# Performance work log

Hardware: AMD Instinct MI355X
Metric: run time of the kernel (lower is better)

## Reference

```python
import jax, jax.numpy as jnp
import numpy as np

IN_FEATURES = 8192
OUT_FEATURES = 8192
POOL_K = 16
SCALE = 2.0


def setup_inputs() -> dict:
    key = jax.random.key(0)
    k1, k2, k3 = jax.random.split(key, 3)
    B = 4096
    x = jax.random.normal(k1, (B, IN_FEATURES), dtype=jnp.float32)
    # nn.Linear default init: U(-1/sqrt(fan_in), 1/sqrt(fan_in))
    bound = 1.0 / np.sqrt(IN_FEATURES)
    W = jax.random.uniform(k2, (OUT_FEATURES, IN_FEATURES), dtype=jnp.float32, minval=-bound, maxval=bound)
    b = jax.random.uniform(k3, (OUT_FEATURES,), dtype=jnp.float32, minval=-bound, maxval=bound)
    return {"x": x, "W": W, "b": b}


def reference(x, W, b):
    # GEMM: [B, C_out]
    y = jnp.dot(x, W.T) + b
    B, C = y.shape
    # AvgPool1d over feature dim, kernel=stride=POOL_K -> [B, C/POOL_K]
    pooled = y.reshape(B, C // POOL_K, POOL_K).mean(axis=-1)
    # GELU (tanh approximation) + scale, then row-wise max -> [B]
    v = jax.nn.gelu(pooled, approximate=True) * SCALE
    return jnp.max(v, axis=-1)
```

## Files before the change

### kernel.cpp

```cpp
#include <hip/hip_runtime.h>
#include <hip/hip_bf16.h>
#include <cmath>

#define M_DIM 4096
#define N_POOL 512
#define K_DIM 8192
#define KSPLIT 4
#define K_PER (K_DIM / KSPLIT)

typedef __bf16 bf16x8 __attribute__((ext_vector_type(8)));
typedef float floatx4 __attribute__((ext_vector_type(4)));

__device__ __forceinline__ unsigned short f2bf(float f) {
  unsigned int u = __float_as_uint(f);
  return (unsigned short)((u + 0x7fffu + ((u >> 16) & 1u)) >> 16);
}

__global__ __launch_bounds__(256) void prep_kernel(
    const float* __restrict__ W, unsigned short* __restrict__ Wp,
    const float* __restrict__ b, float* __restrict__ bpool) {
  int bid = blockIdx.x;
  if (bid < N_POOL) {
    int g = bid;
    const float* base = W + (size_t)g * 16 * K_DIM;
    ushort4* out = (ushort4*)(Wp + (size_t)g * K_DIM);
    for (int c4 = threadIdx.x; c4 < K_DIM / 4; c4 += blockDim.x) {
      float4 s = {0.f, 0.f, 0.f, 0.f};
#pragma unroll
      for (int j = 0; j < 16; ++j) {
        float4 v = ((const float4*)(base + (size_t)j * K_DIM))[c4];
        s.x += v.x; s.y += v.y; s.z += v.z; s.w += v.w;
      }
      ushort4 o;
      o.x = f2bf(s.x); o.y = f2bf(s.y); o.z = f2bf(s.z); o.w = f2bf(s.w);
      out[c4] = o;
    }
  } else {
    for (int g = threadIdx.x; g < N_POOL; g += blockDim.x) {
      float s = 0.f;
#pragma unroll
      for (int i = 0; i < 16; ++i) s += b[g * 16 + i];
      bpool[g] = s;
    }
  }
}

__global__ __launch_bounds__(256) void gemm_splitk(
    const float* __restrict__ x,
    const unsigned short* __restrict__ wp,
    float* __restrict__ part)
{
  __shared__ __align__(16) unsigned short As[128 * 64];
  __shared__ __align__(16) unsigned short Bs[128 * 64];

  const int tid = threadIdx.x;
  const int L = tid & 63;
  const int w = tid >> 6;
  const int wm = w & 1, wn = w >> 1;
  const int lane15 = L & 15, quad = L >> 4;

  const int id = blockIdx.x;
  const int xcd = id & 7;
  const int c = id >> 3;
  const int kz = xcd >> 1;
  const int j = (c << 1) | (xcd & 1);
  const int bn = j & 3, bm = j >> 2;

  const int srow = w * 32 + (L >> 3);
  const int gcol8 = (L & 7) ^ ((L >> 3) & 7);
  const float* gx = x + (size_t)(bm * 128 + srow) * K_DIM + kz * K_PER + gcol8 * 8;
  const unsigned short* gb = wp + (size_t)(bn * 128 + srow) * K_DIM + kz * K_PER + gcol8 * 8;
  unsigned short* wA = As + srow * 64 + (L & 7) * 8;
  unsigned short* lB = Bs + (w * 32) * 64;

  floatx4 acc[4][4];
#pragma unroll
  for (int t = 0; t < 4; ++t)
#pragma unroll
    for (int u = 0; u < 4; ++u) acc[t][u] = (floatx4)0.f;

  const bf16x8* Av = (const bf16x8*)As;
  const bf16x8* Bv = (const bf16x8*)Bs;

  for (int kk = 0; kk < K_PER / 64; ++kk) {
    float4 fa[4], fb4[4];
#pragma unroll
    for (int i = 0; i < 4; ++i) {
      const float4* p = (const float4*)(gx + (size_t)(i * 8) * K_DIM);
      fa[i] = p[0];
      fb4[i] = p[1];
    }
#pragma unroll
    for (int i = 0; i < 4; ++i) {
      __builtin_amdgcn_global_load_lds(
          (const __attribute__((address_space(1))) void*)(gb + (size_t)(i * 8) * K_DIM),
          (__attribute__((address_space(3))) void*)(lB + i * 8 * 64), 16, 0, 0);
    }
    gx += 64; gb += 64;
#pragma unroll
    for (int i = 0; i < 4; ++i) {
      uint4 o;
      asm("v_cvt_pk_bf16_f32 %0, %1, %2" : "=v"(o.x) : "v"(fa[i].x), "v"(fa[i].y));
      asm("v_cvt_pk_bf16_f32 %0, %1, %2" : "=v"(o.y) : "v"(fa[i].z), "v"(fa[i].w));
      asm("v_cvt_pk_bf16_f32 %0, %1, %2" : "=v"(o.z) : "v"(fb4[i].x), "v"(fb4[i].y));
      asm("v_cvt_pk_bf16_f32 %0, %1, %2" : "=v"(o.w) : "v"(fb4[i].z), "v"(fb4[i].w));
      *(uint4*)(wA + (size_t)(i * 8) * 64) = o;
    }
    __syncthreads();

#pragma unroll
    for (int ks = 0; ks < 2; ++ks) {
      bf16x8 af[4], bfr[4];
#pragma unroll
      for (int t = 0; t < 4; ++t) {
        int r = wm * 64 + t * 16 + lane15;
        af[t] = Av[r * 8 + ((ks * 4 + quad) ^ (lane15 & 7))];
      }
#pragma unroll
      for (int u = 0; u < 4; ++u) {
        int r = wn * 64 + u * 16 + lane15;
        bfr[u] = Bv[r * 8 + ((ks * 4 + quad) ^ (lane15 & 7))];
      }
#pragma unroll
      for (int t = 0; t < 4; ++t)
#pragma unroll
        for (int u = 0; u < 4; ++u)
          acc[t][u] = __builtin_amdgcn_mfma_f32_16x16x32_bf16(af[t], bfr[u],
                                                              acc[t][u], 0, 0, 0);
    }
    __syncthreads();
  }

  float* cp = part + (size_t)kz * M_DIM * N_POOL;
  const int row_base = bm * 128 + wm * 64;
  const int col_base = bn * 128 + wn * 64;
#pragma unroll
  for (int t = 0; t < 4; ++t)
#pragma unroll
    for (int u = 0; u < 4; ++u) {
      int col = col_base + u * 16 + lane15;
#pragma unroll
      for (int r = 0; r < 4; ++r) {
        int row = row_base + t * 16 + quad * 4 + r;
        cp[(size_t)row * N_POOL + col] = acc[t][u][r];
      }
    }
}

__device__ __forceinline__ float gelu2(float s) {
  float p = s * 0.0625f;
  float t = tanhf(0.7978845608028654f * (p + 0.044715f * p * p * p));
  return p * (1.0f + t);
}

__global__ void finalize(const float* __restrict__ part,
                         const float* __restrict__ bpool,
                         float* __restrict__ out) {
  const int w = threadIdx.x >> 6, lane = threadIdx.x & 63;
  const int row = blockIdx.x * 4 + w;
  const float4* bp4 = (const float4*)bpool;
  float mx = -INFINITY;
#pragma unroll
  for (int j = 0; j < 2; ++j) {
    int g4 = lane + j * 64;
    float4 s = bp4[g4];
#pragma unroll
    for (int kz = 0; kz < KSPLIT; ++kz) {
      float4 v = ((const float4*)(part + (size_t)kz * M_DIM * N_POOL +
                                  (size_t)row * N_POOL))[g4];
      s.x += v.x; s.y += v.y; s.z += v.z; s.w += v.w;
    }
    mx = fmaxf(mx, fmaxf(fmaxf(gelu2(s.x), gelu2(s.y)),
                         fmaxf(gelu2(s.z), gelu2(s.w))));
  }
#pragma unroll
  for (int sh = 32; sh >= 1; sh >>= 1) mx = fmaxf(mx, __shfl_xor(mx, sh));
  if (lane == 0) out[row] = mx;
}

extern "C" void kernel_launch(void* const* d_in, const int* in_sizes, int n_in,
                              void* d_out, int out_size, void* d_ws, size_t ws_size,
                              hipStream_t stream) {
  const float* x = (const float*)d_in[0];
  const float* W = (const float*)d_in[1];
  const float* b = (const float*)d_in[2];
  float* out = (float*)d_out;

  char* ws = (char*)d_ws;
  unsigned short* Wp = (unsigned short*)ws;
  float* part = (float*)(ws + (size_t)8388608);
  float* bpool = (float*)(ws + (size_t)41943040);

  prep_kernel<<<N_POOL + 1, 256, 0, stream>>>(W, Wp, b, bpool);

  gemm_splitk<<<512, 256, 0, stream>>>(x, Wp, part);

  finalize<<<M_DIM / 4, 256, 0, stream>>>(part, bpool, out);
}
```

Baseline: 475.3 us.

## Double-buffer LDS tiles to overlap global loads with MFMA compute

Splits the shared-memory A and B tiles into two buffers. The next K-slice is fetched (x into registers, W via direct global-to-LDS loads) while MFMAs run on the current buffer, leaving one barrier per iteration. This hides global-load latency behind compute in the split-K GEMM. The cost is double the LDS use (64KB per block) and more live registers, which may lower occupancy.

```diff
diff --git a/kernel.cpp b/kernel.cpp
--- a/kernel.cpp
+++ b/kernel.cpp
@@ -50,8 +50,8 @@
     const unsigned short* __restrict__ wp,
     float* __restrict__ part)
 {
-  __shared__ __align__(16) unsigned short As[128 * 64];
-  __shared__ __align__(16) unsigned short Bs[128 * 64];
+  __shared__ __align__(16) unsigned short As[2][128 * 64];
+  __shared__ __align__(16) unsigned short Bs[2][128 * 64];
 
   const int tid = threadIdx.x;
   const int L = tid & 63;
@@ -70,8 +70,8 @@
   const int gcol8 = (L & 7) ^ ((L >> 3) & 7);
   const float* gx = x + (size_t)(bm * 128 + srow) * K_DIM + kz * K_PER + gcol8 * 8;
   const unsigned short* gb = wp + (size_t)(bn * 128 + srow) * K_DIM + kz * K_PER + gcol8 * 8;
-  unsigned short* wA = As + srow * 64 + (L & 7) * 8;
-  unsigned short* lB = Bs + (w * 32) * 64;
+  const int aoff = srow * 64 + (L & 7) * 8;
+  const int boff = (w * 32) * 64;
 
   floatx4 acc[4][4];
 #pragma unroll
@@ -79,10 +79,7 @@
 #pragma unroll
     for (int u = 0; u < 4; ++u) acc[t][u] = (floatx4)0.f;
 
-  const bf16x8* Av = (const bf16x8*)As;
-  const bf16x8* Bv = (const bf16x8*)Bs;
-
-  for (int kk = 0; kk < K_PER / 64; ++kk) {
+  {
     float4 fa[4], fb4[4];
 #pragma unroll
     for (int i = 0; i < 4; ++i) {
@@ -94,7 +91,7 @@
     for (int i = 0; i < 4; ++i) {
       __builtin_amdgcn_global_load_lds(
           (const __attribute__((address_space(1))) void*)(gb + (size_t)(i * 8) * K_DIM),
-          (__attribute__((address_space(3))) void*)(lB + i * 8 * 64), 16, 0, 0);
+          (__attribute__((address_space(3))) void*)(Bs[0] + boff + i * 8 * 64), 16, 0, 0);
     }
     gx += 64; gb += 64;
 #pragma unroll
@@ -104,10 +101,32 @@
       asm("v_cvt_pk_bf16_f32 %0, %1, %2" : "=v"(o.y) : "v"(fa[i].z), "v"(fa[i].w));
       asm("v_cvt_pk_bf16_f32 %0, %1, %2" : "=v"(o.z) : "v"(fb4[i].x), "v"(fb4[i].y));
       asm("v_cvt_pk_bf16_f32 %0, %1, %2" : "=v"(o.w) : "v"(fb4[i].z), "v"(fb4[i].w));
-      *(uint4*)(wA + (size_t)(i * 8) * 64) = o;
+      *(uint4*)(As[0] + aoff + i * 8 * 64) = o;
     }
     __syncthreads();
-
+  }
+
+  const int NK = K_PER / 64;
+  for (int kk = 0; kk < NK - 1; ++kk) {
+    const int cur = kk & 1, nxt = cur ^ 1;
+
+    float4 na[4], nb[4];
+#pragma unroll
+    for (int i = 0; i < 4; ++i) {
+      const float4* p = (const float4*)(gx + (size_t)(i * 8) * K_DIM);
+      na[i] = p[0];
+      nb[i] = p[1];
+    }
+#pragma unroll
+    for (int i = 0; i < 4; ++i) {
+      __builtin_amdgcn_global_load_lds(
+          (const __attribute__((address_space(1))) void*)(gb + (size_t)(i * 8) * K_DIM),
+          (__attribute__((address_space(3))) void*)(Bs[nxt] + boff + i * 8 * 64), 16, 0, 0);
+    }
+    gx += 64; gb += 64;
+
+    const bf16x8* Av = (const bf16x8*)As[cur];
+    const bf16x8* Bv = (const bf16x8*)Bs[cur];
 #pragma unroll
     for (int ks = 0; ks < 2; ++ks) {
       bf16x8 af[4], bfr[4];
@@ -128,7 +147,43 @@
           acc[t][u] = __builtin_amdgcn_mfma_f32_16x16x32_bf16(af[t], bfr[u],
                                                               acc[t][u], 0, 0, 0);
     }
+
+#pragma unroll
+    for (int i = 0; i < 4; ++i) {
+      uint4 o;
+      asm("v_cvt_pk_bf16_f32 %0, %1, %2" : "=v"(o.x) : "v"(na[i].x), "v"(na[i].y));
+      asm("v_cvt_pk_bf16_f32 %0, %1, %2" : "=v"(o.y) : "v"(na[i].z), "v"(na[i].w));
+      asm("v_cvt_pk_bf16_f32 %0, %1, %2" : "=v"(o.z) : "v"(nb[i].x), "v"(nb[i].y));
+      asm("v_cvt_pk_bf16_f32 %0, %1, %2" : "=v"(o.w) : "v"(nb[i].z), "v"(nb[i].w));
+      *(uint4*)(As[nxt] + aoff + i * 8 * 64) = o;
+    }
     __syncthreads();
+  }
+
+  {
+    const int cur = (NK - 1) & 1;
+    const bf16x8* Av = (const bf16x8*)As[cur];
+    const bf16x8* Bv = (const bf16x8*)Bs[cur];
+#pragma unroll
+    for (int ks = 0; ks < 2; ++ks) {
+      bf16x8 af[4], bfr[4];
+#pragma unroll
+      for (int t = 0; t < 4; ++t) {
+        int r = wm * 64 + t * 16 + lane15;
+        af[t] = Av[r * 8 + ((ks * 4 + quad) ^ (lane15 & 7))];
+      }
+#pragma unroll
+      for (int u = 0; u < 4; ++u) {
+        int r = wn * 64 + u * 16 + lane15;
+        bfr[u] = Bv[r * 8 + ((ks * 4 + quad) ^ (lane15 & 7))];
+      }
+#pragma unroll
+      for (int t = 0; t < 4; ++t)
+#pragma unroll
+        for (int u = 0; u < 4; ++u)
+          acc[t][u] = __builtin_amdgcn_mfma_f32_16x16x32_bf16(af[t], bfr[u],
+                                                              acc[t][u], 0, 0, 0);
+    }
   }
 
   float* cp = part + (size_t)kz * M_DIM * N_POOL;
```

Result: slower. 490.2 us (+3.1%).
